# Kernel tuning notes

Measured on AMD Instinct MI355X. Metric: run time of the kernel, lower is better.

## Reference

```python
import jax, jax.numpy as jnp
import numpy as np

# ---- static config (from xib add_argument defaults / chosen production sizes) ----
B, L = 16, 50            # batch, text length
LU, KU, DIM = 60, 100, 60
V, MAXVL = 2000, 10      # vocab size, max vocab word length (J)
MIN_WL, MAX_WL = 4, 10   # min/max extracted word length
NE = MAX_WL - MIN_WL + 1 # number of len_e candidates
INS_DEL_COST = 3.5       # min_ins_del_cost
UNEXTRACTED_PROB = 0.01
CONTEXT_WEIGHT = 0.1     # weight for context (conv) log-probs
NEG = -9999.9


def setup_inputs() -> dict:
    key = jax.random.key(0)
    ks = jax.random.split(key, 8)
    unit_id_seqs = jax.random.randint(ks[0], (B, L), 0, LU)
    lengths = 10 + jax.random.randint(ks[1], (B,), 0, L - 9)  # in [10, L]
    unit_repr = jax.random.normal(ks[2], (KU, DIM), jnp.float32)
    aligner_weight = 0.1 * jax.random.normal(ks[3], (LU, KU), jnp.float32)
    conv_w = jax.random.normal(ks[4], (DIM, DIM, 3), jnp.float32) / np.sqrt(3.0 * DIM)
    conv_b = jnp.zeros((DIM,), jnp.float32)
    vocab_ids = jax.random.randint(ks[5], (V, MAXVL), 0, KU)
    vocab_lengths = MIN_WL + jax.random.randint(ks[6], (V,), 0, MAXVL - MIN_WL + 1)
    return dict(unit_id_seqs=unit_id_seqs, lengths=lengths, unit_repr=unit_repr,
                aligner_weight=aligner_weight, conv_w=conv_w, conv_b=conv_b,
                vocab_ids=vocab_ids, vocab_lengths=vocab_lengths)


def reference(unit_id_seqs, lengths, unit_repr, aligner_weight, conv_w, conv_b,
              vocab_ids, vocab_lengths):
    # ---- G2P layer: embedding-as-matmul + Conv1d over length ----
    ku_char_repr = aligner_weight @ unit_repr                 # (LU, DIM)
    emb = ku_char_repr[unit_id_seqs]                          # (B, L, DIM)
    x = jnp.swapaxes(emb, 1, 2)                               # (B, DIM, L)
    y = jax.lax.conv_general_dilated(x, conv_w, (1,), 'SAME',
                                     dimension_numbers=('NCH', 'OIH', 'NCH'))
    word_repr = jnp.swapaxes(y + conv_b[None, :, None], 1, 2)  # (B, L, DIM)
    char_log_probs = jax.nn.log_softmax(ku_char_repr @ unit_repr.T, axis=-1)  # (LU, KU)
    alignment = jnp.exp(char_log_probs)
    ctx_log_probs = jax.nn.log_softmax(word_repr @ unit_repr.T, axis=-1)      # (B, L, KU)
    # per-position substitution log prob against each known unit
    pos_lp = char_log_probs[unit_id_seqs] + CONTEXT_WEIGHT * ctx_log_probs    # (B, L, KU)
    sub = pos_lp[:, :, vocab_ids]                                             # (B, L, V, J)
    sub = jnp.pad(sub, ((0, 0), (0, MAX_WL), (0, 0), (0, 0)), constant_values=NEG)
    J = MAXVL
    # ---- edit-distance style DP over (span char i, vocab char j), vectorized
    # over (batch, start position, vocab). prev[b,s,j,v] = f[i-1][j].
    j_ar = jnp.arange(J + 1, dtype=sub.dtype)
    prev = jnp.broadcast_to((-INS_DEL_COST * j_ar)[None, None, :, None], (B, L, J + 1, V))
    vl_idx = jnp.broadcast_to(vocab_lengths[None, None, None, :].astype(jnp.int32), (B, L, 1, V))
    lls = []
    for i in range(1, MAX_WL + 1):          # fixed small loop (<=10)
        sub_i = sub[:, i - 1:i - 1 + L]     # (B, L, V, J): char at position s+i-1
        row = [jnp.full((B, L, V), -INS_DEL_COST * i, dtype=sub.dtype)]
        for j in range(1, J + 1):           # fixed small loop (<=10)
            diag = prev[:, :, j - 1, :] + sub_i[:, :, :, j - 1]
            up = prev[:, :, j, :] - INS_DEL_COST
            left = row[j - 1] - INS_DEL_COST
            row.append(jnp.maximum(diag, jnp.maximum(up, left)))
        prev = jnp.stack(row, axis=2)       # (B, L, J+1, V)
        if i >= MIN_WL:                     # matched ll for word length i
            lls.append(jnp.take_along_axis(prev, vl_idx, axis=2)[:, :, 0, :])
    ll = jnp.stack(lls, axis=2)             # (B, L, NE, V) = matches.ll
    # ---- viability mask + unextracted penalty, pick best candidate ----
    starts = jnp.arange(L)
    word_lens = MIN_WL + jnp.arange(NE)
    viable = (starts[None, :, None] + word_lens[None, None, :]) <= lengths[:, None, None]  # (B,L,NE)
    unextracted = (lengths[:, None, None] - word_lens[None, None, :]).astype(ll.dtype)     # (B,1,NE)
    score = (ll + jnp.where(viable, 0.0, NEG)[..., None]
             + (unextracted * np.log(UNEXTRACTED_PROB))[..., None, :, None][:, 0])
    flat = score.reshape(B, L * NE * V)
    best_idx = jnp.argmax(flat, axis=1)
    best_matched_ll = jnp.max(flat, axis=1)
    start = best_idx // (NE * V)
    e_idx = (best_idx // V) % NE
    best_matched_vocab = best_idx % V
    end = start + MIN_WL + e_idx - 1
    return start, end, best_matched_ll, best_matched_vocab, alignment
```

## Files before the change

### kernel.cpp

```cpp
#include <hip/hip_runtime.h>
#include <math.h>
#include <stdint.h>

#define B_ 16
#define L_ 50
#define LU_ 60
#define KU_ 100
#define DIM_ 60
#define V_ 2000
#define MAXVL_ 10
#define MIN_WL_ 4
#define MAX_WL_ 10
#define NE_ 7
#define IDC_ 3.5f
#define LOG_UNEXT_ (-4.6051701859880913680359829093687f)
#define CTXW_ 0.1f

#define WS_KU   0
#define WS_CLP  3600
#define WS_PLP  9600
#define WS_BEST_BYTES (89600u * 4u)
#define BEST_STRIDE 8

#define URP_ 61
#define CWP_ 61
#define TSP_ 12

__global__ __launch_bounds__(128) void prep_kernel(
    const float* __restrict__ unit_repr,
    const float* __restrict__ aligner_weight,
    float* __restrict__ ws_f,
    unsigned long long* __restrict__ g_best,
    float* __restrict__ out_align)
{
  __shared__ float s_ur[KU_ * URP_];
  __shared__ float s_aw[KU_];
  __shared__ float s_ku[DIM_];
  __shared__ float s_lg[KU_];
  __shared__ float sred[128];
  int r = blockIdx.x;
  int t = threadIdx.x;
  if (r == 0 && t < B_) g_best[t * BEST_STRIDE] = 0ull;
  for (int i = t; i < KU_ * DIM_; i += 128)
    s_ur[(i / DIM_) * URP_ + (i % DIM_)] = unit_repr[i];
  if (t < KU_) s_aw[t] = aligner_weight[r * KU_ + t];
  __syncthreads();
  if (t < DIM_) {
    float acc = 0.f;
    for (int k = 0; k < KU_; ++k) acc += s_aw[k] * s_ur[k * URP_ + t];
    s_ku[t] = acc;
    ws_f[WS_KU + r * DIM_ + t] = acc;
  }
  __syncthreads();
  if (t < KU_) {
    float acc = 0.f;
    for (int d = 0; d < DIM_; ++d) acc += s_ku[d] * s_ur[t * URP_ + d];
    s_lg[t] = acc;
  }
  __syncthreads();
  sred[t] = (t < KU_) ? s_lg[t] : -1e30f;
  __syncthreads();
  for (int off = 64; off > 0; off >>= 1) {
    if (t < off) sred[t] = fmaxf(sred[t], sred[t + off]);
    __syncthreads();
  }
  float m = sred[0];
  __syncthreads();
  sred[t] = (t < KU_) ? expf(s_lg[t] - m) : 0.f;
  __syncthreads();
  for (int off = 64; off > 0; off >>= 1) {
    if (t < off) sred[t] += sred[t + off];
    __syncthreads();
  }
  float ls = m + logf(sred[0]);
  if (t < KU_) {
    float lp = s_lg[t] - ls;
    ws_f[WS_CLP + r * KU_ + t] = lp;
    out_align[r * KU_ + t] = expf(lp);
  }
}

__global__ __launch_bounds__(256) void ctx_kernel(
    const int* __restrict__ uid,
    const float* __restrict__ unit_repr,
    const float* __restrict__ conv_w,
    const float* __restrict__ conv_b,
    const float* __restrict__ ws_f,
    float* __restrict__ ws_plp)
{
  int bl = blockIdx.x;
  int b = bl / L_, l = bl % L_;
  int t = threadIdx.x;
  __shared__ float s_ur[KU_ * URP_];
  __shared__ float s_cw[3 * DIM_ * CWP_];
  __shared__ float sx[3 * DIM_];
  __shared__ float swr[DIM_];
  __shared__ float slog[KU_];
  __shared__ float sred[256];

  const float4* ur4 = (const float4*)unit_repr;
  for (int k = t; k < (KU_ * DIM_) / 4; k += 256) {
    float4 v = ur4[k];
    int i0 = 4 * k;
    s_ur[((i0 + 0) / DIM_) * URP_ + ((i0 + 0) % DIM_)] = v.x;
    s_ur[((i0 + 1) / DIM_) * URP_ + ((i0 + 1) % DIM_)] = v.y;
    s_ur[((i0 + 2) / DIM_) * URP_ + ((i0 + 2) % DIM_)] = v.z;
    s_ur[((i0 + 3) / DIM_) * URP_ + ((i0 + 3) % DIM_)] = v.w;
  }
  const float4* cw4 = (const float4*)conv_w;
  for (int k = t; k < (DIM_ * DIM_ * 3) / 4; k += 256) {
    float4 v = cw4[k];
    int i0 = 4 * k;
    float vv[4] = {v.x, v.y, v.z, v.w};
#pragma unroll
    for (int e = 0; e < 4; ++e) {
      int idx = i0 + e;
      int o = idx / (3 * DIM_), id = idx % (3 * DIM_);
      s_cw[id * CWP_ + o] = vv[e];
    }
  }
  if (t < 3 * DIM_) {
    int d = t / DIM_, c = t % DIM_;
    int ld = l + d - 1;
    float vv = 0.f;
    if (ld >= 0 && ld < L_) {
      int u = uid[b * L_ + ld];
      vv = ws_f[WS_KU + u * DIM_ + c];
    }
    sx[t] = vv;
  }
  __syncthreads();
  if (t < DIM_) {
    float acc = conv_b[t];
    for (int i = 0; i < DIM_; ++i) {
      acc += sx[0 * DIM_ + i] * s_cw[(i * 3 + 0) * CWP_ + t];
      acc += sx[1 * DIM_ + i] * s_cw[(i * 3 + 1) * CWP_ + t];
      acc += sx[2 * DIM_ + i] * s_cw[(i * 3 + 2) * CWP_ + t];
    }
    swr[t] = acc;
  }
  __syncthreads();
  if (t < KU_) {
    float acc = 0.f;
    for (int d = 0; d < DIM_; ++d) acc += swr[d] * s_ur[t * URP_ + d];
    slog[t] = acc;
  }
  __syncthreads();
  sred[t] = (t < KU_) ? slog[t] : -1e30f;
  __syncthreads();
  for (int off = 128; off > 0; off >>= 1) {
    if (t < off) sred[t] = fmaxf(sred[t], sred[t + off]);
    __syncthreads();
  }
  float m = sred[0];
  __syncthreads();
  sred[t] = (t < KU_) ? expf(slog[t] - m) : 0.f;
  __syncthreads();
  for (int off = 128; off > 0; off >>= 1) {
    if (t < off) sred[t] += sred[t + off];
    __syncthreads();
  }
  float ls = m + logf(sred[0]);
  if (t < KU_) {
    int u = uid[b * L_ + l];
    float lp = slog[t] - ls;
    ws_plp[bl * KU_ + t] = ws_f[WS_CLP + u * KU_ + t] + CTXW_ * lp;
  }
}

__global__ __launch_bounds__(256) void dp_kernel(
    const int* __restrict__ lengths,
    const int* __restrict__ vocab_ids,
    const int* __restrict__ vocab_lengths,
    const float* __restrict__ ws_plp,
    unsigned long long* __restrict__ g_best)
{
  int bl = blockIdx.x;
  int b = bl / L_, l = bl % L_;
  int len_b = lengths[b];
  int imax = len_b - l;
  if (imax > MAX_WL_) imax = MAX_WL_;
  if (imax < MIN_WL_) return;

  __shared__ float sT[KU_ * TSP_];
  __shared__ unsigned long long swave[4];
  int t = threadIdx.x;
  {
    int n = imax * KU_;
    for (int idx = t; idx < n; idx += 256) {
      int i = idx / KU_, k = idx - i * KU_;
      sT[k * TSP_ + i] = ws_plp[(bl + i) * KU_ + k];
    }
  }
  __syncthreads();

  int v0 = blockIdx.y * 512 + t;
  int v1 = v0 + 256;
  bool has1 = (v1 < V_);
  int vid0[MAXVL_], vid1[MAXVL_];
#pragma unroll
  for (int j = 0; j < MAXVL_; ++j) vid0[j] = vocab_ids[v0 * MAXVL_ + j];
  if (has1) {
#pragma unroll
    for (int j = 0; j < MAXVL_; ++j) vid1[j] = vocab_ids[v1 * MAXVL_ + j];
  } else {
#pragma unroll
    for (int j = 0; j < MAXVL_; ++j) vid1[j] = 0;
  }
  int vlen0 = vocab_lengths[v0];
  int vlen1 = has1 ? vocab_lengths[v1] : MIN_WL_;

  float A0[MAXVL_ + 1], A1[MAXVL_ + 1];
  float sv0[NE_], sv1[NE_];
#pragma unroll
  for (int e = 0; e < NE_; ++e) { sv0[e] = 0.f; sv1[e] = 0.f; }
#pragma unroll
  for (int i = 0; i <= MAXVL_; ++i) {
    A0[i] = -IDC_ * (float)i;
    A1[i] = A0[i];
  }

#pragma unroll
  for (int j = 1; j <= MAXVL_; ++j) {
    const float* c0 = &sT[vid0[j - 1] * TSP_];
    const float* c1 = &sT[vid1[j - 1] * TSP_];
    float4 a0 = *(const float4*)(c0);
    float4 m0 = *(const float4*)(c0 + 4);
    float2 e0 = *(const float2*)(c0 + 8);
    float4 a1 = *(const float4*)(c1);
    float4 m1 = *(const float4*)(c1 + 4);
    float2 e1 = *(const float2*)(c1 + 8);
    float s0[MAXVL_] = {a0.x, a0.y, a0.z, a0.w, m0.x, m0.y, m0.z, m0.w, e0.x, e0.y};
    float s1[MAXVL_] = {a1.x, a1.y, a1.z, a1.w, m1.x, m1.y, m1.z, m1.w, e1.x, e1.y};
    float B0[MAXVL_ + 1], B1[MAXVL_ + 1];
    B0[0] = -IDC_ * (float)j;
    B1[0] = B0[0];
#pragma unroll
    for (int i = 1; i <= MAXVL_; ++i) {
      B0[i] = fmaxf(A0[i - 1] + s0[i - 1], fmaxf(A0[i], B0[i - 1]) - IDC_);
      B1[i] = fmaxf(A1[i - 1] + s1[i - 1], fmaxf(A1[i], B1[i - 1]) - IDC_);
    }
    if (j == vlen0) {
#pragma unroll
      for (int e = 0; e < NE_; ++e) sv0[e] = B0[MIN_WL_ + e];
    }
    if (j == vlen1) {
#pragma unroll
      for (int e = 0; e < NE_; ++e) sv1[e] = B1[MIN_WL_ + e];
    }
#pragma unroll
    for (int i = 0; i <= MAXVL_; ++i) { A0[i] = B0[i]; A1[i] = B1[i]; }
  }

  unsigned long long bestKey = 0ull;
#pragma unroll
  for (int e = 0; e < NE_; ++e) {
    int i = MIN_WL_ + e;
    if (i <= imax) {
      float unext = (float)(len_b - i) * LOG_UNEXT_;
      unsigned int idx_base = (unsigned int)(l * (NE_ * V_) + e * V_);
      {
        float score = sv0[e] + unext;
        unsigned int u = __float_as_uint(score);
        u = (u & 0x80000000u) ? ~u : (u | 0x80000000u);
        unsigned long long key =
            ((unsigned long long)u << 32) |
            (unsigned long long)(~(idx_base + (unsigned int)v0));
        if (key > bestKey) bestKey = key;
      }
      if (has1) {
        float score = sv1[e] + unext;
        unsigned int u = __float_as_uint(score);
        u = (u & 0x80000000u) ? ~u : (u | 0x80000000u);
        unsigned long long key =
            ((unsigned long long)u << 32) |
            (unsigned long long)(~(idx_base + (unsigned int)v1));
        if (key > bestKey) bestKey = key;
      }
    }
  }

#pragma unroll
  for (int off = 32; off > 0; off >>= 1) {
    unsigned long long o = __shfl_down(bestKey, off);
    if (o > bestKey) bestKey = o;
  }
  int wid = t >> 6;
  if ((t & 63) == 0) swave[wid] = bestKey;
  __syncthreads();
  if (t == 0) {
    unsigned long long k0 = swave[0];
    for (int w = 1; w < 4; ++w)
      if (swave[w] > k0) k0 = swave[w];
    atomicMax(g_best + (size_t)b * BEST_STRIDE, k0);
  }
}

__global__ void decode_kernel(const unsigned long long* __restrict__ g_best,
                              float* __restrict__ out)
{
  int t = threadIdx.x;
  if (t < B_) {
    unsigned long long key = g_best[t * BEST_STRIDE];
    unsigned int u = (unsigned int)(key >> 32);
    unsigned int idx = ~((unsigned int)(key & 0xFFFFFFFFull));
    unsigned int bits = (u & 0x80000000u) ? (u & 0x7FFFFFFFu) : ~u;
    float val = __uint_as_float(bits);
    int start = (int)(idx / (NE_ * V_));
    int rem = (int)(idx % (NE_ * V_));
    int e = rem / V_;
    int vv = rem % V_;
    out[t] = (float)start;
    out[B_ + t] = (float)(start + MIN_WL_ + e - 1);
    out[2 * B_ + t] = val;
    out[3 * B_ + t] = (float)vv;
  }
}

extern "C" void kernel_launch(void* const* d_in, const int* in_sizes, int n_in,
                              void* d_out, int out_size, void* d_ws, size_t ws_size,
                              hipStream_t stream)
{
  const int* uid            = (const int*)d_in[0];
  const int* lengths        = (const int*)d_in[1];
  const float* unit_repr    = (const float*)d_in[2];
  const float* aligner_w    = (const float*)d_in[3];
  const float* conv_w       = (const float*)d_in[4];
  const float* conv_b       = (const float*)d_in[5];
  const int* vocab_ids      = (const int*)d_in[6];
  const int* vocab_lengths  = (const int*)d_in[7];
  float* out = (float*)d_out;
  float* ws_f = (float*)d_ws;
  unsigned long long* g_best =
      (unsigned long long*)((char*)d_ws + WS_BEST_BYTES);

  prep_kernel<<<LU_, 128, 0, stream>>>(unit_repr, aligner_w, ws_f, g_best,
                                       out + 4 * B_);
  ctx_kernel<<<B_ * L_, 256, 0, stream>>>(uid, unit_repr, conv_w, conv_b, ws_f,
                                          ws_f + WS_PLP);
  dim3 g3(B_ * L_, 4);
  dp_kernel<<<g3, 256, 0, stream>>>(lengths, vocab_ids, vocab_lengths,
                                    ws_f + WS_PLP, g_best);
  decode_kernel<<<1, 64, 0, stream>>>(g_best, out);
}
```

Measured before the change: 111.9 us.

## Fuse prep kernel into ctx kernel and use wave-shuffle log-softmax reductions

```diff
diff --git a/kernel.cpp b/kernel.cpp
--- a/kernel.cpp
+++ b/kernel.cpp
@@ -16,87 +16,39 @@
 #define LOG_UNEXT_ (-4.6051701859880913680359829093687f)
 #define CTXW_ 0.1f
 
-#define WS_KU   0
-#define WS_CLP  3600
-#define WS_PLP  9600
-#define WS_BEST_BYTES (89600u * 4u)
+#define WS_PLP  0
+#define WS_BEST_BYTES (80000u * 4u)
 #define BEST_STRIDE 8
 
 #define URP_ 61
 #define CWP_ 61
 #define TSP_ 12
 
-__global__ __launch_bounds__(128) void prep_kernel(
-    const float* __restrict__ unit_repr,
-    const float* __restrict__ aligner_weight,
-    float* __restrict__ ws_f,
-    unsigned long long* __restrict__ g_best,
-    float* __restrict__ out_align)
-{
-  __shared__ float s_ur[KU_ * URP_];
-  __shared__ float s_aw[KU_];
-  __shared__ float s_ku[DIM_];
-  __shared__ float s_lg[KU_];
-  __shared__ float sred[128];
-  int r = blockIdx.x;
-  int t = threadIdx.x;
-  if (r == 0 && t < B_) g_best[t * BEST_STRIDE] = 0ull;
-  for (int i = t; i < KU_ * DIM_; i += 128)
-    s_ur[(i / DIM_) * URP_ + (i % DIM_)] = unit_repr[i];
-  if (t < KU_) s_aw[t] = aligner_weight[r * KU_ + t];
-  __syncthreads();
-  if (t < DIM_) {
-    float acc = 0.f;
-    for (int k = 0; k < KU_; ++k) acc += s_aw[k] * s_ur[k * URP_ + t];
-    s_ku[t] = acc;
-    ws_f[WS_KU + r * DIM_ + t] = acc;
-  }
-  __syncthreads();
-  if (t < KU_) {
-    float acc = 0.f;
-    for (int d = 0; d < DIM_; ++d) acc += s_ku[d] * s_ur[t * URP_ + d];
-    s_lg[t] = acc;
-  }
-  __syncthreads();
-  sred[t] = (t < KU_) ? s_lg[t] : -1e30f;
-  __syncthreads();
-  for (int off = 64; off > 0; off >>= 1) {
-    if (t < off) sred[t] = fmaxf(sred[t], sred[t + off]);
-    __syncthreads();
-  }
-  float m = sred[0];
-  __syncthreads();
-  sred[t] = (t < KU_) ? expf(s_lg[t] - m) : 0.f;
-  __syncthreads();
-  for (int off = 64; off > 0; off >>= 1) {
-    if (t < off) sred[t] += sred[t + off];
-    __syncthreads();
-  }
-  float ls = m + logf(sred[0]);
-  if (t < KU_) {
-    float lp = s_lg[t] - ls;
-    ws_f[WS_CLP + r * KU_ + t] = lp;
-    out_align[r * KU_ + t] = expf(lp);
-  }
-}
-
 __global__ __launch_bounds__(256) void ctx_kernel(
     const int* __restrict__ uid,
     const float* __restrict__ unit_repr,
+    const float* __restrict__ aligner_w,
     const float* __restrict__ conv_w,
     const float* __restrict__ conv_b,
-    const float* __restrict__ ws_f,
-    float* __restrict__ ws_plp)
+    float* __restrict__ ws_plp,
+    float* __restrict__ out_align,
+    unsigned long long* __restrict__ g_best)
 {
   int bl = blockIdx.x;
   int b = bl / L_, l = bl % L_;
   int t = threadIdx.x;
   __shared__ float s_ur[KU_ * URP_];
   __shared__ float s_cw[3 * DIM_ * CWP_];
+  __shared__ float s_aw[3 * KU_];
   __shared__ float sx[3 * DIM_];
+  __shared__ float s_kur[DIM_];
   __shared__ float swr[DIM_];
+  __shared__ float sclp[KU_];
   __shared__ float slog[KU_];
-  __shared__ float sred[256];
+  __shared__ float salg[KU_];
+  __shared__ float sls[3];
+
+  if (bl == 0 && t < B_) g_best[t * BEST_STRIDE] = 0ull;
 
   const float4* ur4 = (const float4*)unit_repr;
   for (int k = t; k < (KU_ * DIM_) / 4; k += 256) {
@@ -119,17 +71,31 @@
       s_cw[id * CWP_ + o] = vv[e];
     }
   }
+  int ud[3];
+#pragma unroll
+  for (int d = 0; d < 3; ++d) {
+    int ld = l + d - 1;
+    ud[d] = (ld >= 0 && ld < L_) ? uid[b * L_ + ld] : -1;
+  }
+  for (int i = t; i < 3 * KU_; i += 256) {
+    int d = i / KU_, k = i - d * KU_;
+    s_aw[i] = (ud[d] >= 0) ? aligner_w[ud[d] * KU_ + k] : 0.f;
+  }
+  __syncthreads();
+
   if (t < 3 * DIM_) {
-    int d = t / DIM_, c = t % DIM_;
-    int ld = l + d - 1;
-    float vv = 0.f;
-    if (ld >= 0 && ld < L_) {
-      int u = uid[b * L_ + ld];
-      vv = ws_f[WS_KU + u * DIM_ + c];
-    }
-    sx[t] = vv;
-  }
-  __syncthreads();
+    int d = t / DIM_, c = t - d * DIM_;
+    float acc = 0.f;
+    for (int k = 0; k < KU_; ++k) acc += s_aw[d * KU_ + k] * s_ur[k * URP_ + c];
+    sx[t] = acc;
+  } else if (bl < LU_ && t >= 192 && t < 192 + DIM_) {
+    int c = t - 192;
+    float acc = 0.f;
+    for (int k = 0; k < KU_; ++k) acc += aligner_w[bl * KU_ + k] * s_ur[k * URP_ + c];
+    s_kur[c] = acc;
+  }
+  __syncthreads();
+
   if (t < DIM_) {
     float acc = conv_b[t];
     for (int i = 0; i < DIM_; ++i) {
@@ -138,33 +104,50 @@
       acc += sx[2 * DIM_ + i] * s_cw[(i * 3 + 2) * CWP_ + t];
     }
     swr[t] = acc;
-  }
-  __syncthreads();
+  } else if (t >= 64 && t < 64 + KU_) {
+    int j = t - 64;
+    float acc = 0.f;
+    for (int d = 0; d < DIM_; ++d) acc += sx[DIM_ + d] * s_ur[j * URP_ + d];
+    sclp[j] = acc;
+  }
+  __syncthreads();
+
   if (t < KU_) {
     float acc = 0.f;
     for (int d = 0; d < DIM_; ++d) acc += swr[d] * s_ur[t * URP_ + d];
     slog[t] = acc;
-  }
-  __syncthreads();
-  sred[t] = (t < KU_) ? slog[t] : -1e30f;
-  __syncthreads();
-  for (int off = 128; off > 0; off >>= 1) {
-    if (t < off) sred[t] = fmaxf(sred[t], sred[t + off]);
-    __syncthreads();
-  }
-  float m = sred[0];
-  __syncthreads();
-  sred[t] = (t < KU_) ? expf(slog[t] - m) : 0.f;
-  __syncthreads();
-  for (int off = 128; off > 0; off >>= 1) {
-    if (t < off) sred[t] += sred[t + off];
-    __syncthreads();
-  }
-  float ls = m + logf(sred[0]);
+  } else if (bl < LU_ && t >= 128 && t < 128 + KU_) {
+    int j = t - 128;
+    float acc = 0.f;
+    for (int d = 0; d < DIM_; ++d) acc += s_kur[d] * s_ur[j * URP_ + d];
+    salg[j] = acc;
+  }
+  __syncthreads();
+
+  {
+    int w = t >> 6, lane = t & 63;
+    int nred = (bl < LU_) ? 3 : 2;
+    if (w < nred) {
+      const float* arr = (w == 0) ? sclp : (w == 1) ? slog : salg;
+      float v1 = arr[lane];
+      float v2 = (lane < KU_ - 64) ? arr[64 + lane] : -1e30f;
+      float mx = fmaxf(v1, v2);
+#pragma unroll
+      for (int off = 32; off > 0; off >>= 1)
+        mx = fmaxf(mx, __shfl_xor(mx, off));
+      float s = expf(v1 - mx) + ((lane < KU_ - 64) ? expf(v2 - mx) : 0.f);
+#pragma unroll
+      for (int off = 32; off > 0; off >>= 1)
+        s += __shfl_xor(s, off);
+      if (lane == 0) sls[w] = mx + logf(s);
+    }
+  }
+  __syncthreads();
+
   if (t < KU_) {
-    int u = uid[b * L_ + l];
-    float lp = slog[t] - ls;
-    ws_plp[bl * KU_ + t] = ws_f[WS_CLP + u * KU_ + t] + CTXW_ * lp;
+    float pos = (sclp[t] - sls[0]) + CTXW_ * (slog[t] - sls[1]);
+    ws_plp[bl * KU_ + t] = pos;
+    if (bl < LU_) out_align[bl * KU_ + t] = expf(salg[t] - sls[2]);
   }
 }
 
@@ -209,6 +192,7 @@
   }
   int vlen0 = vocab_lengths[v0];
   int vlen1 = has1 ? vocab_lengths[v1] : MIN_WL_;
+  bool tail = (imax > 8);
 
   float A0[MAXVL_ + 1], A1[MAXVL_ + 1];
   float sv0[NE_], sv1[NE_];
@@ -226,10 +210,13 @@
     const float* c1 = &sT[vid1[j - 1] * TSP_];
     float4 a0 = *(const float4*)(c0);
     float4 m0 = *(const float4*)(c0 + 4);
-    float2 e0 = *(const float2*)(c0 + 8);
     float4 a1 = *(const float4*)(c1);
     float4 m1 = *(const float4*)(c1 + 4);
-    float2 e1 = *(const float2*)(c1 + 8);
+    float2 e0 = make_float2(0.f, 0.f), e1 = make_float2(0.f, 0.f);
+    if (tail) {
+      e0 = *(const float2*)(c0 + 8);
+      e1 = *(const float2*)(c1 + 8);
+    }
     float s0[MAXVL_] = {a0.x, a0.y, a0.z, a0.w, m0.x, m0.y, m0.z, m0.w, e0.x, e0.y};
     float s1[MAXVL_] = {a1.x, a1.y, a1.z, a1.w, m1.x, m1.y, m1.z, m1.w, e1.x, e1.y};
     float B0[MAXVL_ + 1], B1[MAXVL_ + 1];
@@ -334,10 +321,9 @@
   unsigned long long* g_best =
       (unsigned long long*)((char*)d_ws + WS_BEST_BYTES);
 
-  prep_kernel<<<LU_, 128, 0, stream>>>(unit_repr, aligner_w, ws_f, g_best,
-                                       out + 4 * B_);
-  ctx_kernel<<<B_ * L_, 256, 0, stream>>>(uid, unit_repr, conv_w, conv_b, ws_f,
-                                          ws_f + WS_PLP);
+  ctx_kernel<<<B_ * L_, 256, 0, stream>>>(uid, unit_repr, aligner_w, conv_w,
+                                          conv_b, ws_f + WS_PLP, out + 4 * B_,
+                                          g_best);
   dim3 g3(B_ * L_, 4);
   dp_kernel<<<g3, 256, 0, stream>>>(lengths, vocab_ids, vocab_lengths,
                                     ws_f + WS_PLP, g_best);
```

After: 118.1 us. 5.6% more time.
